# Performance work log

Hardware: AMD Instinct MI355X
Metric: run time of the kernel (lower is better)

The kernel has to match this reference:

```python
import jax, jax.numpy as jnp
import numpy as np

B, N, E, H = 2, 4096, 1024, 16
HD = E // H                      # head_dim = 64
R = 8                            # LoRA rank
LORA_SCALE = 16.0 / R            # alpha / r = 2.0
BUCKET_SIZES = (256, 64, 16)


def setup_inputs() -> dict:
    key = jax.random.key(0)
    ks = jax.random.split(key, 24)
    inp = {"x": jax.random.normal(ks[0], (B, N, E), jnp.float32)}
    inp["wb_coarse"] = jax.random.randint(ks[1], (B, N), 0, 16)
    inp["wb_mid"] = jax.random.randint(ks[2], (B, N), 0, 64)
    inp["wb_fine"] = jax.random.randint(ks[3], (B, N), 0, 256)
    i = 4
    for name in ("q", "k", "v", "o"):
        inp[f"W{name}"] = jax.random.normal(ks[i], (E, E), jnp.float32) / np.sqrt(E); i += 1
        inp[f"b{name}"] = jax.random.normal(ks[i], (E,), jnp.float32) * 0.01; i += 1
        inp[f"A{name}"] = jax.random.normal(ks[i], (R, E), jnp.float32) / np.sqrt(E); i += 1
        inp[f"B{name}"] = jax.random.normal(ks[i], (E, R), jnp.float32) * 0.01; i += 1
    return inp


def _lora(x, W, b, A, Bm):
    # F.linear(x, W, b) + scale * x @ A.T @ B.T   (dropout=0 in eval)
    return x @ W.T + b + LORA_SCALE * ((x @ A.T) @ Bm.T)


def _chunked_attn(q, k, v, bidx, C):
    # q,k,v: [BH, N, D]; bidx: [BH, N] int; C: chunk size (divides N)
    BH, Nn, D = q.shape
    sidx = jnp.argsort(bidx, axis=1)
    uidx = jnp.argsort(sidx, axis=1)
    g = lambda t, i: jnp.take_along_axis(t, i[..., None], axis=1)
    qs, ks_, vs = g(q, sidx), g(k, sidx), g(v, sidx)
    nc = Nn // C
    qs = qs.reshape(BH, nc, C, D)
    ks_ = ks_.reshape(BH, nc, C, D)
    vs = vs.reshape(BH, nc, C, D)
    # previous chunk (look-back of one chunk); chunk 0 has no previous -> masked
    k_prev = jnp.concatenate([jnp.zeros_like(ks_[:, :1]), ks_[:, :-1]], axis=1)
    v_prev = jnp.concatenate([jnp.zeros_like(vs[:, :1]), vs[:, :-1]], axis=1)
    k_cat = jnp.concatenate([k_prev, ks_], axis=2)   # [BH, nc, 2C, D]
    v_cat = jnp.concatenate([v_prev, vs], axis=2)
    scores = jnp.einsum('bncd,bnkd->bnck', qs, k_cat) / jnp.sqrt(jnp.asarray(D, qs.dtype))
    # mask look-back keys for chunk 0 (torch path attends only within chunk 0)
    chunk_ids = jnp.arange(nc)[:, None, None]        # [nc,1,1]
    key_pos = jnp.arange(2 * C)[None, None, :]       # [1,1,2C]
    neg = jnp.finfo(scores.dtype).min
    scores = jnp.where((chunk_ids == 0) & (key_pos < C), neg, scores)
    attn = jax.nn.softmax(scores, axis=-1)
    out = jnp.einsum('bnck,bnkd->bncd', attn, v_cat).reshape(BH, Nn, D)
    return jnp.take_along_axis(out, uidx[..., None], axis=1)


def reference(x, wb_coarse, wb_mid, wb_fine,
              Wq, bq, Aq, Bq, Wk, bk, Ak, Bk,
              Wv, bv, Av, Bv, Wo, bo, Ao, Bo):
    q = _lora(x, Wq, bq, Aq, Bq)
    k = _lora(x, Wk, bk, Ak, Bk)
    v = _lora(x, Wv, bv, Av, Bv)
    to_heads = lambda t: t.reshape(B, N, H, HD).transpose(0, 2, 1, 3).reshape(B * H, N, HD)
    qh, kh, vh = to_heads(q), to_heads(k), to_heads(v)
    expand = lambda w: jnp.broadcast_to(w[:, None, :], (B, H, N)).reshape(B * H, N)
    wbs = (expand(wb_coarse), expand(wb_mid), expand(wb_fine))
    outs = (_chunked_attn(qh, kh, vh, wbs[0], BUCKET_SIZES[0])
            + _chunked_attn(qh, kh, vh, wbs[1], BUCKET_SIZES[1])
            + _chunked_attn(qh, kh, vh, wbs[2], BUCKET_SIZES[2])) / 3.0
    outs = outs.reshape(B, H, N, HD).transpose(0, 2, 1, 3).reshape(B, N, E)
    return _lora(outs, Wo, bo, Ao, Bo)
```

## Files before the change

kernel.cpp:

```cpp
#include <hip/hip_runtime.h>
#include <cstdint>
#include <cstddef>

#define BDIM 2
#define NTOK 4096
#define EDIM 1024
#define HEADS 16
#define HDIM 64
#define MROWS (BDIM * NTOK)

typedef unsigned short u16;
typedef __attribute__((ext_vector_type(8))) short bf16x8;
typedef __attribute__((ext_vector_type(8))) unsigned short u16x8;
typedef __attribute__((ext_vector_type(4))) float f32x4;

#define MFMA(a, b, c) __builtin_amdgcn_mfma_f32_16x16x32_bf16(a, b, c, 0, 0, 0)
#define BAR() asm volatile("s_barrier" ::: "memory")
#define SETPRIO(p) __builtin_amdgcn_s_setprio(p)

__device__ inline void split2(float x, u16& h, u16& l) {
    union { float f; unsigned u; } a;
    a.f = x;
    unsigned uh = a.u + 0x7fff + ((a.u >> 16) & 1);
    h = (u16)(uh >> 16);
    union { unsigned u; float f; } hf; hf.u = (unsigned)h << 16;
    a.f = x - hf.f;
    unsigned ul = a.u + 0x7fff + ((a.u >> 16) & 1);
    l = (u16)(ul >> 16);
}

__device__ inline u16 bf16rne(float x) {
    union { float f; unsigned u; } a; a.f = x;
    unsigned r = a.u + 0x7fff + ((a.u >> 16) & 1);
    return (u16)(r >> 16);
}

#define GLL(gp, lp) __builtin_amdgcn_global_load_lds( \
    (const __attribute__((address_space(1))) unsigned*)(gp), \
    (__attribute__((address_space(3))) unsigned*)(lp), 16, 0, 0)

__global__ __launch_bounds__(256) void build_weff4_kernel(
    const float* __restrict__ W0, const float* __restrict__ A0, const float* __restrict__ B0,
    const float* __restrict__ W1, const float* __restrict__ A1, const float* __restrict__ B1,
    const float* __restrict__ W2, const float* __restrict__ A2, const float* __restrict__ B2,
    const float* __restrict__ W3, const float* __restrict__ A3, const float* __restrict__ B3,
    u16* __restrict__ dh0, u16* __restrict__ dl0,
    u16* __restrict__ dh1, u16* __restrict__ dl1,
    u16* __restrict__ dh2, u16* __restrict__ dl2,
    u16* __restrict__ dh3, u16* __restrict__ dl3)
{
    int s = blockIdx.y;
    const float* W = (s == 0) ? W0 : (s == 1) ? W1 : (s == 2) ? W2 : W3;
    const float* A = (s == 0) ? A0 : (s == 1) ? A1 : (s == 2) ? A2 : A3;
    const float* Bm = (s == 0) ? B0 : (s == 1) ? B1 : (s == 2) ? B2 : B3;
    u16* dh = (s == 0) ? dh0 : (s == 1) ? dh1 : (s == 2) ? dh2 : dh3;
    u16* dl = (s == 0) ? dl0 : (s == 1) ? dl1 : (s == 2) ? dl2 : dl3;

    int idx = blockIdx.x * 256 + threadIdx.x;
    int o = idx >> 10, i = idx & 1023;
    float sum = 0.f;
#pragma unroll
    for (int r = 0; r < 8; ++r) sum += Bm[o * 8 + r] * A[r * 1024 + i];
    float w = W[idx] + 2.0f * sum;
    u16 h, l;
    split2(w, h, l);
    dh[idx] = h; dl[idx] = l;
}

__global__ __launch_bounds__(256) void split_kernel(
    const float* __restrict__ src, u16* __restrict__ dh, u16* __restrict__ dl)
{
    int idx = blockIdx.x * 256 + threadIdx.x;
    float4 v = ((const float4*)src)[idx];
    ushort4 h, l;
    split2(v.x, h.x, l.x);
    split2(v.y, h.y, l.y);
    split2(v.z, h.z, l.z);
    split2(v.w, h.w, l.w);
    ((ushort4*)dh)[idx] = h;
    ((ushort4*)dl)[idx] = l;
}

__global__ __launch_bounds__(256) void sumsplit3_kernel(
    const float* __restrict__ A, const float* __restrict__ B,
    const float* __restrict__ Cc, u16* __restrict__ dh, u16* __restrict__ dl)
{
    int idx = blockIdx.x * 256 + threadIdx.x;
    float4 a = ((const float4*)A)[idx];
    float4 b = ((const float4*)B)[idx];
    float4 c = ((const float4*)Cc)[idx];
    float v[4] = {(a.x + b.x) + c.x, (a.y + b.y) + c.y,
                  (a.z + b.z) + c.z, (a.w + b.w) + c.w};
    ushort4 h, l;
    split2(v[0], h.x, l.x);
    split2(v[1], h.y, l.y);
    split2(v[2], h.z, l.z);
    split2(v[3], h.w, l.w);
    ((ushort4*)dh)[idx] = h;
    ((ushort4*)dl)[idx] = l;
}

__global__ __launch_bounds__(256) void sort3_kernel(
    const int* __restrict__ w0, const int* __restrict__ w1,
    const int* __restrict__ w2, int* __restrict__ sidx)
{
    __shared__ int sb[NTOK];
    __shared__ int cnt[32][256];
    __shared__ int gb[256];
    const int* srcs[3] = {w0, w1, w2};
    int t = threadIdx.x;
    const int* w = srcs[blockIdx.y] + blockIdx.x * NTOK;
    int* outp = sidx + ((int)blockIdx.y * BDIM + (int)blockIdx.x) * NTOK;

    for (int i = t; i < NTOK; i += 256) sb[i] = w[i];
    for (int i = t; i < 32 * 256; i += 256) ((int*)cnt)[i] = 0;
    __syncthreads();

    int g = t >> 3;
#pragma unroll
    for (int e = 0; e < 16; ++e)
        atomicAdd(&cnt[g][sb[g * 128 + (t & 7) + 8 * e]], 1);
    __syncthreads();

    int run = 0;
#pragma unroll
    for (int gg = 0; gg < 32; ++gg) {
        int c = cnt[gg][t];
        cnt[gg][t] = run;
        run += c;
    }
    gb[t] = run;
    __syncthreads();
    if (t == 0) {
        int acc = 0;
        for (int v = 0; v < 256; ++v) { int c = gb[v]; gb[v] = acc; acc += c; }
    }
    __syncthreads();
    for (int i = t; i < 32 * 256; i += 256) {
        int v = i & 255, gg = i >> 8;
        cnt[gg][v] += gb[v];
    }
    __syncthreads();

    if (t < 32) {
        int base = t * 128;
        for (int e = 0; e < 128; ++e) {
            int v = sb[base + e];
            int p = cnt[t][v]++;
            outp[p] = base + e;
        }
    }
}

__global__ __launch_bounds__(512, 2) void gemm_qk_kernel(
    const u16* __restrict__ Xh, const u16* __restrict__ Xl,
    const u16* __restrict__ Wh, const u16* __restrict__ Wl,
    const float* __restrict__ bq, const float* __restrict__ bk,
    u16* __restrict__ qh, u16* __restrict__ ql,
    u16* __restrict__ kh, u16* __restrict__ kl)
{
    __shared__ __align__(16) unsigned char smem[147456];
    u16* lds = (u16*)smem;
    const int PA_h = 0, PA_l = 8192, PB_h = 16384, PB_l = 20480;

    int t = threadIdx.x;
    int lane = t & 63, wave = t >> 6;
    int bid = blockIdx.x;
    int wg = (bid & 7) * 64 + (bid >> 3);
    int bx = wg & 15, by = wg >> 4;
    int m0 = by * 256, n0 = bx * 128;

    int lrow = lane & 15, lq = lane >> 4;
    size_t aoff = (size_t)(m0 + wave * 32 + lrow) * EDIM + lq * 8;
    size_t boff = (size_t)(n0 + wave * 16 + lrow) * EDIM + lq * 8;
    int slabA = wave * 2;
    int sA0 = (wave >> 1) * 4;
    int sB0 = (wave & 1) * 4;
    f32x4 acc[4][4] = {};

#pragma unroll
    for (int tt = 0; tt < 2; ++tt) {
        u16* sbuf = lds + tt * 24576;
        int kk = tt * 32;
        GLL(Xh + aoff + kk,             sbuf + PA_h + (slabA + 0) * 512);
        GLL(Xh + aoff + kk + 16 * EDIM, sbuf + PA_h + (slabA + 1) * 512);
        GLL(Xl + aoff + kk,             sbuf + PA_l + (slabA + 0) * 512);
        GLL(Xl + aoff + kk + 16 * EDIM, sbuf + PA_l + (slabA + 1) * 512);
        GLL(Wh + boff + kk, sbuf + PB_h + wave * 512);
        GLL(Wl + boff + kk, sbuf + PB_l + wave * 512);
    }
    asm volatile("s_waitcnt vmcnt(6)" ::: "memory");
    BAR();

    for (int t32 = 0; t32 < 32; ++t32) {
        u16* rb = lds + (t32 % 3) * 24576;
        u16* sbuf = lds + ((t32 + 2) % 3) * 24576;
        bool pf = (t32 + 2) < 32;
        int kn = (t32 + 2) * 32;
        bf16x8 bhf[4], blf[4];
#pragma unroll
        for (int p = 0; p < 4; ++p) {
            if (p == 0) {
// ... 4 lines not shown
                }
            }
            bf16x8 aph = *(const bf16x8*)(rb + PA_h + (sA0 + p) * 512 + lane * 8);
            bf16x8 apl = *(const bf16x8*)(rb + PA_l + (sA0 + p) * 512 + lane * 8);
            if (pf) {
                if (p == 0) {
                    GLL(Xh + aoff + kn,             sbuf + PA_h + (slabA + 0) * 512);
                    GLL(Xh + aoff + kn + 16 * EDIM, sbuf + PA_h + (slabA + 1) * 512);
                } else if (p == 1) {
                    GLL(Xl + aoff + kn,             sbuf + PA_l + (slabA + 0) * 512);
                    GLL(Xl + aoff + kn + 16 * EDIM, sbuf + PA_l + (slabA + 1) * 512);
                } else if (p == 2) {
                    GLL(Wh + boff + kn, sbuf + PB_h + wave * 512);
                    GLL(Wl + boff + kn, sbuf + PB_l + wave * 512);
                }
            }
            BAR();
            SETPRIO(1);
#pragma unroll
            for (int j = 0; j < 4; ++j) {
                acc[p][j] = MFMA(aph, bhf[j], acc[p][j]);
                acc[p][j] = MFMA(aph, blf[j], acc[p][j]);
                acc[p][j] = MFMA(apl, bhf[j], acc[p][j]);
            }
            SETPRIO(0);
            if (p == 3) {
                if (pf) asm volatile("s_waitcnt vmcnt(6)" ::: "memory");
                else    asm volatile("s_waitcnt vmcnt(0)" ::: "memory");
            }
            BAR();
        }
    }

    int proj = n0 >> 10;
    const float* bias = proj ? bk : bq;
    u16* ohp = proj ? kh : qh;
    u16* olp = proj ? kl : ql;
    int wm = (wave >> 1) * 64, wn = (wave & 1) * 64;
    int q4 = lane >> 4, l16 = lane & 15;
    int cb = (n0 & 1023) + wn;
    float bj[4];
#pragma unroll
    for (int j = 0; j < 4; ++j) bj[j] = bias[cb + j * 16 + l16];
    float* repw = (float*)smem + wave * 2176;
    int r8 = lane >> 3, c8 = lane & 7;
#pragma unroll
    for (int gph = 0; gph < 2; ++gph) {
#pragma unroll
        for (int ii = 0; ii < 2; ++ii)
#pragma unroll
            for (int j = 0; j < 4; ++j)
#pragma unroll
                for (int r = 0; r < 4; ++r)
                    repw[(ii * 16 + q4 * 4 + r) * 68 + j * 16 + l16] =
                        acc[gph * 2 + ii][j][r] + bj[j];
#pragma unroll
        for (int rg = 0; rg < 4; ++rg) {
            int lr = rg * 8 + r8;
            float4 f0 = *(float4*)(repw + lr * 68 + c8 * 8);
            float4 f1 = *(float4*)(repw + lr * 68 + c8 * 8 + 4);
            float fa[8] = {f0.x, f0.y, f0.z, f0.w, f1.x, f1.y, f1.z, f1.w};
            size_t off = (size_t)(m0 + wm + gph * 32 + lr) * EDIM + cb + c8 * 8;
            u16x8 hv, lv;
#pragma unroll
            for (int e = 0; e < 8; ++e) {
                float v = fa[e];
                if (proj == 0) v *= 0.125f;
                u16 hh, ll;
                split2(v, hh, ll);
                hv[e] = hh; lv[e] = ll;
            }
            *(u16x8*)(ohp + off) = hv;
            *(u16x8*)(olp + off) = lv;
        }
    }
}

__global__ __launch_bounds__(512, 2) void gemm_v_kernel(
    const u16* __restrict__ Xh, const u16* __restrict__ Wv,
    const float* __restrict__ bv, u16* __restrict__ vh)
{
    __shared__ __align__(16) unsigned char smem[73728];
    u16* lds = (u16*)smem;

    int t = threadIdx.x;
    int lane = t & 63, wave = t >> 6;
    int bid = blockIdx.x;
    int wg = (bid & 7) * 32 + (bid >> 3);
    int bx = wg & 7, by = wg >> 3;
    int m0 = by * 256, nc0 = bx * 128;

    int lrow = lane & 15, lq = lane >> 4;
    size_t aoff = (size_t)(m0 + wave * 32 + lrow) * EDIM + lq * 8;
    size_t boff = (size_t)(nc0 + wave * 16 + lrow) * EDIM + lq * 8;
    int slabA = wave * 2;
    int sA0 = (wave >> 1) * 4;
    int sB0 = (wave & 1) * 4;
    f32x4 acc[4][4] = {};

#pragma unroll
    for (int tt = 0; tt < 2; ++tt) {
        u16* sbuf = lds + tt * 12288;
        int kk = tt * 32;
        GLL(Xh + aoff + kk,             sbuf + (slabA + 0) * 512);
        GLL(Xh + aoff + kk + 16 * EDIM, sbuf + (slabA + 1) * 512);
        GLL(Wv + boff + kk,             sbuf + 8192 + wave * 512);
    }
    asm volatile("s_waitcnt vmcnt(3)" ::: "memory");
    BAR();

    for (int t32 = 0; t32 < 32; ++t32) {
        u16* rb = lds + (t32 % 3) * 12288;
        u16* sbuf = lds + ((t32 + 2) % 3) * 12288;
        bool pf = (t32 + 2) < 32;
        int kn = (t32 + 2) * 32;

        bf16x8 bhf[4];
#pragma unroll
        for (int j = 0; j < 4; ++j)
            bhf[j] = *(const bf16x8*)(rb + 8192 + (sB0 + j) * 512 + lane * 8);
        bf16x8 a0 = *(const bf16x8*)(rb + (sA0 + 0) * 512 + lane * 8);
        bf16x8 a1 = *(const bf16x8*)(rb + (sA0 + 1) * 512 + lane * 8);
        if (pf) {
            GLL(Xh + aoff + kn,             sbuf + (slabA + 0) * 512);
            GLL(Xh + aoff + kn + 16 * EDIM, sbuf + (slabA + 1) * 512);
        }
        BAR();
        SETPRIO(1);
#pragma unroll
        for (int j = 0; j < 4; ++j) {
            acc[0][j] = MFMA(a0, bhf[j], acc[0][j]);
            acc[1][j] = MFMA(a1, bhf[j], acc[1][j]);
        }
        SETPRIO(0);
        BAR();

        bf16x8 a2 = *(const bf16x8*)(rb + (sA0 + 2) * 512 + lane * 8);
        bf16x8 a3 = *(const bf16x8*)(rb + (sA0 + 3) * 512 + lane * 8);
        if (pf) GLL(Wv + boff + kn, sbuf + 8192 + wave * 512);
        BAR();
        SETPRIO(1);
#pragma unroll
        for (int j = 0; j < 4; ++j) {
            acc[2][j] = MFMA(a2, bhf[j], acc[2][j]);
            acc[3][j] = MFMA(a3, bhf[j], acc[3][j]);
        }
        SETPRIO(0);
        if (pf) asm volatile("s_waitcnt vmcnt(3)" ::: "memory");
        else    asm volatile("s_waitcnt vmcnt(0)" ::: "memory");
        BAR();
    }

    int wm = (wave >> 1) * 64, wn = (wave & 1) * 64;
    int q4 = lane >> 4, l16 = lane & 15;
    int cb = nc0 + wn;
    float bj[4];
#pragma unroll
    for (int j = 0; j < 4; ++j) bj[j] = bv[cb + j * 16 + l16];
    float* repw = (float*)smem + wave * 2176;
    int r8 = lane >> 3, c8 = lane & 7;
#pragma unroll
    for (int gph = 0; gph < 2; ++gph) {
#pragma unroll
        for (int ii = 0; ii < 2; ++ii)
#pragma unroll
            for (int j = 0; j < 4; ++j)
#pragma unroll
                for (int r = 0; r < 4; ++r)
                    repw[(ii * 16 + q4 * 4 + r) * 68 + j * 16 + l16] =
                        acc[gph * 2 + ii][j][r] + bj[j];
#pragma unroll
        for (int rg = 0; rg < 4; ++rg) {
            int lr = rg * 8 + r8;
            float4 f0 = *(float4*)(repw + lr * 68 + c8 * 8);
            float4 f1 = *(float4*)(repw + lr * 68 + c8 * 8 + 4);
            float fa[8] = {f0.x, f0.y, f0.z, f0.w, f1.x, f1.y, f1.z, f1.w};
            size_t off = (size_t)(m0 + wm + gph * 32 + lr) * EDIM + cb + c8 * 8;
            u16x8 hv;
#pragma unroll
            for (int e = 0; e < 8; ++e) hv[e] = bf16rne(fa[e]);
            *(u16x8*)(vh + off) = hv;
        }
    }
}

__global__ __launch_bounds__(512, 2) void gemm_o_kernel(
    const u16* __restrict__ Xh, const u16* __restrict__ Xl,
    const u16* __restrict__ Wh, const u16* __restrict__ Wl,
    const float* __restrict__ bias, float* __restrict__ Y)
{
    __shared__ __align__(16) unsigned char smem[147456];
    u16* lds = (u16*)smem;
    const int PA_h = 0, PA_l = 8192, PB_h = 16384, PB_l = 20480;

    int t = threadIdx.x;
    int lane = t & 63, wave = t >> 6;
    int bid = blockIdx.x;
    int wg = (bid & 7) * 32 + (bid >> 3);
    int bx = wg & 7, by = wg >> 3;
    int m0 = by * 256, n0 = bx * 128;

    int lrow = lane & 15, lq = lane >> 4;
    size_t aoff = (size_t)(m0 + wave * 32 + lrow) * EDIM + lq * 8;
    size_t boff = (size_t)(n0 + wave * 16 + lrow) * EDIM + lq * 8;
    int slabA = wave * 2;
    int sA0 = (wave >> 1) * 4;
    int sB0 = (wave & 1) * 4;
    f32x4 acc[4][4] = {};

#pragma unroll
    for (int tt = 0; tt < 2; ++tt) {
        u16* sbuf = lds + tt * 24576;
        int kk = tt * 32;
        GLL(Xh + aoff + kk,             sbuf + PA_h + (slabA + 0) * 512);
        GLL(Xh + aoff + kk + 16 * EDIM, sbuf + PA_h + (slabA + 1) * 512);
        GLL(Xl + aoff + kk,             sbuf + PA_l + (slabA + 0) * 512);
        GLL(Xl + aoff + kk + 16 * EDIM, sbuf + PA_l + (slabA + 1) * 512);
        GLL(Wh + boff + kk, sbuf + PB_h + wave * 512);
        GLL(Wl + boff + kk, sbuf + PB_l + wave * 512);
    }
    asm volatile("s_waitcnt vmcnt(6)" ::: "memory");
    BAR();

    for (int t32 = 0; t32 < 32; ++t32) {
        u16* rb = lds + (t32 % 3) * 24576;
        u16* sbuf = lds + ((t32 + 2) % 3) * 24576;
        bool pf = (t32 + 2) < 32;
        int kn = (t32 + 2) * 32;
        bf16x8 bhf[4], blf[4];
#pragma unroll
        for (int p = 0; p < 4; ++p) {
            if (p == 0) {
#pragma unroll
                for (int j = 0; j < 4; ++j) {
                    bhf[j] = *(const bf16x8*)(rb + PB_h + (sB0 + j) * 512 + lane * 8);
                    blf[j] = *(const bf16x8*)(rb + PB_l + (sB0 + j) * 512 + lane * 8);
                }
            }
            bf16x8 aph = *(const bf16x8*)(rb + PA_h + (sA0 + p) * 512 + lane * 8);
            bf16x8 apl = *(const bf16x8*)(rb + PA_l + (sA0 + p) * 512 + lane * 8);
            if (pf) {
                if (p == 0) {
                    GLL(Xh + aoff + kn,             sbuf + PA_h + (slabA + 0) * 512);
                    GLL(Xh + aoff + kn + 16 * EDIM, sbuf + PA_h + (slabA + 1) * 512);
                } else if (p == 1) {
                    GLL(Xl + aoff + kn,             sbuf + PA_l + (slabA + 0) * 512);
                    GLL(Xl + aoff + kn + 16 * EDIM, sbuf + PA_l + (slabA + 1) * 512);
                } else if (p == 2) {
                    GLL(Wh + boff + kn, sbuf + PB_h + wave * 512);
                    GLL(Wl + boff + kn, sbuf + PB_l + wave * 512);
                }
            }
            BAR();
            SETPRIO(1);
#pragma unroll
            for (int j = 0; j < 4; ++j) {
                acc[p][j] = MFMA(aph, bhf[j], acc[p][j]);
                acc[p][j] = MFMA(aph, blf[j], acc[p][j]);
                acc[p][j] = MFMA(apl, bhf[j], acc[p][j]);
            }
            SETPRIO(0);
            if (p == 3) {
                if (pf) asm volatile("s_waitcnt vmcnt(6)" ::: "memory");
                else    asm volatile("s_waitcnt vmcnt(0)" ::: "memory");
            }
            BAR();
        }
    }

    int wm = (wave >> 1) * 64, wn = (wave & 1) * 64;
    int col_in = lane & 15, rquad = lane >> 4;
#pragma unroll
    for (int j = 0; j < 4; ++j) {
        int col = n0 + wn + j * 16 + col_in;
        float bvv = bias[col];
#pragma unroll
        for (int i = 0; i < 4; ++i) {
            int mbase = m0 + wm + i * 16 + rquad * 4;
#pragma unroll
            for (int r = 0; r < 4; ++r)
                Y[(size_t)(mbase + r) * EDIM + col] = acc[i][j][r] + bvv;
        }
    }
}

template <int MODE>
__global__ __launch_bounds__(256, 3) void attn_mfma_kernel(
    const u16* __restrict__ Qh, const u16* __restrict__ Ql,
    const u16* __restrict__ Kh, const u16* __restrict__ Kl,
    const u16* __restrict__ Vh, const int* __restrict__ sidx_base, int zofs,
    float* __restrict__ out0, float* __restrict__ out1, float* __restrict__ out2,
    u16* __restrict__ osh, u16* __restrict__ osl)
{
    __shared__ u16 KfH[2][4096], KfL[2][4096];
    __shared__ u16 VL[64 * 72];
    __shared__ u16 PbH[4 * 16 * 56];

    int bx_, bh_, bz_;
    if (MODE == 0 && gridDim.z == 3) {
        int lid = blockIdx.x + (blockIdx.y << 5) + (blockIdx.z << 10);
        int xcd = lid & 7, j = lid >> 3;
        bh_ = xcd + 8 * (j / 96);
        int rem = j % 96;
        bz_ = rem >> 5;
        bx_ = rem & 31;
    } else {
        bx_ = blockIdx.x; bh_ = blockIdx.y; bz_ = blockIdx.z;
    }

    int sidx_i = bz_ + zofs;
    int lgC = 8 - 2 * sidx_i;
    const int* sxb = sidx_base + sidx_i * BDIM * NTOK;
    float* out = (sidx_i == 0) ? out0 : (sidx_i == 1) ? out1 : out2;

    int t = threadIdx.x;
    int lane = t & 63, wave = t >> 6;
    int quad = lane >> 4, l16 = lane & 15;
    int b = bh_ >> 4, h = bh_ & 15;
    int p0 = bx_ * 128;
    sxb += b * NTOK;

    int ptile[2], ws_[2], we_[2];
    bf16x8 qhf[2][2], qlf[2][2];
#pragma unroll
    for (int tq = 0; tq < 2; ++tq) {
        ptile[tq] = p0 + wave * 32 + tq * 16;
        int c = ptile[tq] >> lgC;
        ws_[tq] = (c > 0) ? (c - 1) << lgC : 0;
        we_[tq] = (c + 1) << lgC;
// ... 101 lines not shown
                        sa = MFMA(qhf[tq][1], kl0[1], sa);
                        sa = MFMA(qlf[tq][1], kh0[1], sa);
                    }
                    if (v1) {
                        sb2 = MFMA(qhf[tq][0], kh1[0], sb2);
                        sb2 = MFMA(qhf[tq][0], kl1[0], sb2);
                        sb2 = MFMA(qlf[tq][0], kh1[0], sb2);
                        sb2 = MFMA(qhf[tq][1], kh1[1], sb2);
                        sb2 = MFMA(qhf[tq][1], kl1[1], sb2);
                        sb2 = MFMA(qlf[tq][1], kh1[1], sb2);
                    }
                    SETPRIO(0);
                    float smax = -1e30f;
                    if (v0) smax = fmaxf(smax, fmaxf(fmaxf(sa[0], sa[1]), fmaxf(sa[2], sa[3])));
                    if (v1) smax = fmaxf(smax, fmaxf(fmaxf(sb2[0], sb2[1]), fmaxf(sb2[2], sb2[3])));
                    smax = fmaxf(smax, __shfl_xor(smax, 1));
                    smax = fmaxf(smax, __shfl_xor(smax, 2));
                    smax = fmaxf(smax, __shfl_xor(smax, 4));
                    smax = fmaxf(smax, __shfl_xor(smax, 8));
                    float mold = mrun[tq];
                    float mnew = mold;
                    if (smax > mold + 8.0f) {
                        mnew = smax;
                        mrun[tq] = mnew;
                        float alpha = __expf(mold - mnew);
#pragma unroll
                        for (int r = 0; r < 4; ++r) lpart[tq][r] *= alpha;
#pragma unroll
                        for (int dt = 0; dt < 4; ++dt) {
                            oacc[tq][dt][0] *= alpha; oacc[tq][dt][1] *= alpha;
                            oacc[tq][dt][2] *= alpha; oacc[tq][dt][3] *= alpha;
                        }
                    }
                    u16* pbh = PbH + wave * 896;
#pragma unroll
                    for (int r = 0; r < 4; ++r) {
                        float pa = v0 ? __expf(sa[r] - mnew) : 0.f;
                        float pbv = v1 ? __expf(sb2[r] - mnew) : 0.f;
                        lpart[tq][r] += pa + pbv;
                        pbh[(quad * 4 + r) * 56 + l16] = bf16rne(pa);
                        pbh[(quad * 4 + r) * 56 + 16 + l16] = bf16rne(pbv);
                    }
                    bf16x8 ph = *(const bf16x8*)(pbh + l16 * 56 + quad * 8);
                    int kh2 = g0 >> 5;
                    SETPRIO(1);
#pragma unroll
                    for (int dt = 0; dt < 4; ++dt) {
                        bf16x8 vv = *(const bf16x8*)(VL + (dt * 16 + l16) * 72 + kh2 * 32 + quad * 8);
                        oacc[tq][dt] = MFMA(ph, vv, oacc[tq][dt]);
                    }
                    SETPRIO(0);
                }
            }
        }

        asm volatile("s_waitcnt vmcnt(0)" ::: "memory");
        __syncthreads();
        if (pf) {
#pragma unroll
            for (int it = 0; it < 2; ++it) {
                int c = it * 256 + t;
                int key = c & 63, dg = c >> 6;
#pragma unroll
                for (int e = 0; e < 8; ++e)
                    VL[(dg * 8 + e) * 72 + key] = (u16)vreg[it][e];
            }
        }
        __syncthreads();
        pb ^= 1;
    }

#pragma unroll
    for (int tq = 0; tq < 2; ++tq) {
        float inv[4];
#pragma unroll
        for (int r = 0; r < 4; ++r) {
// ... 38 lines not shown
    const int*   wbc = (const int*)d_in[1];
    const int*   wbm = (const int*)d_in[2];
    const int*   wbf = (const int*)d_in[3];
    const float* Wq = (const float*)d_in[4],  *bq = (const float*)d_in[5];
    const float* Aq = (const float*)d_in[6],  *Bq = (const float*)d_in[7];
    const float* Wk = (const float*)d_in[8],  *bk = (const float*)d_in[9];
    const float* Ak = (const float*)d_in[10], *Bk = (const float*)d_in[11];
    const float* Wv = (const float*)d_in[12], *bv = (const float*)d_in[13];
    const float* Av = (const float*)d_in[14], *Bv = (const float*)d_in[15];
    const float* Wo = (const float*)d_in[16], *bo = (const float*)d_in[17];
    const float* Ao = (const float*)d_in[18], *Bo = (const float*)d_in[19];

    const size_t EE  = (size_t)EDIM * EDIM;
    const size_t BNE = (size_t)MROWS * EDIM;

    char* wsb = (char*)d_ws;
    float* ab = (float*)wsb;                        wsb += BNE * 4;
    u16* xh = (u16*)wsb;                            wsb += BNE * 2;
    u16* xl = (u16*)wsb;                            wsb += BNE * 2;
    u16* qh = (u16*)wsb;                            wsb += BNE * 2;
    u16* ql = (u16*)wsb;                            wsb += BNE * 2;
    u16* kh = (u16*)wsb;                            wsb += BNE * 2;
    u16* kl = (u16*)wsb;                            wsb += BNE * 2;
    u16* vh = (u16*)wsb;                            wsb += BNE * 2;
    u16* wh_all = (u16*)wsb;                        wsb += 3 * EE * 2;
    u16* wl_all = (u16*)wsb;                        wsb += 3 * EE * 2;
    u16* woh = (u16*)wsb;                           wsb += EE * 2;
    u16* wol = (u16*)wsb;                           wsb += EE * 2;
    int* sidx = (int*)wsb;                          wsb += 3 * BDIM * NTOK * 4;
    float* abC = (float*)wsb;
    size_t need3 = (size_t)(wsb - (char*)d_ws) + BNE * 4;
    bool merged = (ws_size >= need3);

    split_kernel<<<BNE / 1024, 256, 0, stream>>>(x, xh, xl);

    build_weff4_kernel<<<dim3(4096, 4), 256, 0, stream>>>(
        Wq, Aq, Bq, Wk, Ak, Bk, Wv, Av, Bv, Wo, Ao, Bo,
        wh_all + 0 * EE, wl_all + 0 * EE,
        wh_all + 1 * EE, wl_all + 1 * EE,
        wh_all + 2 * EE, wl_all + 2 * EE,
        woh, wol);

    sort3_kernel<<<dim3(BDIM, 3), 256, 0, stream>>>(wbc, wbm, wbf, sidx);

    gemm_qk_kernel<<<512, 512, 0, stream>>>(xh, xl, wh_all, wl_all,
                                            bq, bk, qh, ql, kh, kl);
    gemm_v_kernel<<<256, 512, 0, stream>>>(xh, wh_all + 2 * EE, bv, vh);

    if (merged) {
        float* abB = (float*)xh;
        dim3 ga3(NTOK / 128, BDIM * HEADS, 3);
        attn_mfma_kernel<0><<<ga3, 256, 0, stream>>>(
            qh, ql, kh, kl, vh, sidx, 0, ab, abB, abC, nullptr, nullptr);
        sumsplit3_kernel<<<BNE / 1024, 256, 0, stream>>>(ab, abB, abC, qh, ql);
        gemm_o_kernel<<<256, 512, 0, stream>>>(qh, ql, woh, wol, bo, (float*)d_out);
    } else {
        dim3 ga(NTOK / 128, BDIM * HEADS);
        attn_mfma_kernel<0><<<ga, 256, 0, stream>>>(
            qh, ql, kh, kl, vh, sidx, 0, ab, ab, ab, nullptr, nullptr);
        attn_mfma_kernel<1><<<ga, 256, 0, stream>>>(
            qh, ql, kh, kl, vh, sidx, 1, ab, ab, ab, nullptr, nullptr);
        attn_mfma_kernel<2><<<ga, 256, 0, stream>>>(
            qh, ql, kh, kl, vh, sidx, 2, ab, ab, ab, xh, xl);
        gemm_o_kernel<<<256, 512, 0, stream>>>(xh, xl, woh, wol, bo, (float*)d_out);
    }
}
```

Before: 477.3 us.

## Merge prep kernels and QK/V GEMMs into single launches; pad per-tile P buffer

Folds the x split, LoRA weight build and bucket sort into one prep kernel dispatched by block index, and fuses the Q/K split-precision GEMM and the V GEMM into one launch. The intent is to cut launch overhead and let the sort blocks and the V tiles run alongside the other work instead of serialising, and to reduce tail effects. The attention kernel's P staging buffer is resized to give each tq its own slot with a 40-element row stride, which changes the LDS bank mapping and removes reuse of one buffer across tq. The fused GEMM kernel carries the larger register and LDS footprint of the Q/K path for the V blocks too, and V blocks scheduled first may unbalance work.

Result: no change. 469.2 us, median of 2 (-1.7%).

```diff
diff --git a/kernel.cpp b/kernel.cpp
--- a/kernel.cpp
+++ b/kernel.cpp
@@ -39,7 +39,10 @@
     (const __attribute__((address_space(1))) unsigned*)(gp), \
     (__attribute__((address_space(3))) unsigned*)(lp), 16, 0, 0)
 
-__global__ __launch_bounds__(256) void build_weff4_kernel(
+__global__ __launch_bounds__(256) void prep_kernel(
+    const float* __restrict__ x, u16* __restrict__ xh, u16* __restrict__ xl,
+    const int* __restrict__ w0, const int* __restrict__ w1,
+    const int* __restrict__ w2, int* __restrict__ sidx,
     const float* __restrict__ W0, const float* __restrict__ A0, const float* __restrict__ B0,
     const float* __restrict__ W1, const float* __restrict__ A1, const float* __restrict__ B1,
     const float* __restrict__ W2, const float* __restrict__ A2, const float* __restrict__ B2,
@@ -49,36 +52,85 @@
     u16* __restrict__ dh2, u16* __restrict__ dl2,
     u16* __restrict__ dh3, u16* __restrict__ dl3)
 {
-    int s = blockIdx.y;
-    const float* W = (s == 0) ? W0 : (s == 1) ? W1 : (s == 2) ? W2 : W3;
-    const float* A = (s == 0) ? A0 : (s == 1) ? A1 : (s == 2) ? A2 : A3;
-    const float* Bm = (s == 0) ? B0 : (s == 1) ? B1 : (s == 2) ? B2 : B3;
-    u16* dh = (s == 0) ? dh0 : (s == 1) ? dh1 : (s == 2) ? dh2 : dh3;
-    u16* dl = (s == 0) ? dl0 : (s == 1) ? dl1 : (s == 2) ? dl2 : dl3;
-
-    int idx = blockIdx.x * 256 + threadIdx.x;
-    int o = idx >> 10, i = idx & 1023;
-    float sum = 0.f;
-#pragma unroll
-    for (int r = 0; r < 8; ++r) sum += Bm[o * 8 + r] * A[r * 1024 + i];
-    float w = W[idx] + 2.0f * sum;
-    u16 h, l;
-    split2(w, h, l);
-    dh[idx] = h; dl[idx] = l;
-}
-
-__global__ __launch_bounds__(256) void split_kernel(
-    const float* __restrict__ src, u16* __restrict__ dh, u16* __restrict__ dl)
-{
-    int idx = blockIdx.x * 256 + threadIdx.x;
-    float4 v = ((const float4*)src)[idx];
-    ushort4 h, l;
-    split2(v.x, h.x, l.x);
-    split2(v.y, h.y, l.y);
-    split2(v.z, h.z, l.z);
-    split2(v.w, h.w, l.w);
-    ((ushort4*)dh)[idx] = h;
-    ((ushort4*)dl)[idx] = l;
+    __shared__ int sb[NTOK];
+    __shared__ int cnt[32][256];
+    __shared__ int gb[256];
+    int bid = blockIdx.x;
+    int t = threadIdx.x;
+
+    if (bid < 6) {
+        int by = bid >> 1, bx = bid & 1;
+        const int* srcs[3] = {w0, w1, w2};
+        const int* w = srcs[by] + bx * NTOK;
+        int* outp = sidx + ((int)by * BDIM + (int)bx) * NTOK;
+
+        for (int i = t; i < NTOK; i += 256) sb[i] = w[i];
+        for (int i = t; i < 32 * 256; i += 256) ((int*)cnt)[i] = 0;
+        __syncthreads();
+
+        int g = t >> 3;
+#pragma unroll
+        for (int e = 0; e < 16; ++e)
+            atomicAdd(&cnt[g][sb[g * 128 + (t & 7) + 8 * e]], 1);
+        __syncthreads();
+
+        int run = 0;
+#pragma unroll
+        for (int gg = 0; gg < 32; ++gg) {
+            int c = cnt[gg][t];
+            cnt[gg][t] = run;
+            run += c;
+        }
+        gb[t] = run;
+        __syncthreads();
+        if (t == 0) {
+            int acc = 0;
+            for (int v = 0; v < 256; ++v) { int c = gb[v]; gb[v] = acc; acc += c; }
+        }
+        __syncthreads();
+        for (int i = t; i < 32 * 256; i += 256) {
+            int v = i & 255, gg = i >> 8;
+            cnt[gg][v] += gb[v];
+        }
+        __syncthreads();
+
+        if (t < 32) {
+            int base = t * 128;
+            for (int e = 0; e < 128; ++e) {
+                int v = sb[base + e];
+                int p = cnt[t][v]++;
+                outp[p] = base + e;
+            }
+        }
+    } else if (bid < 8198) {
+        int idx = (bid - 6) * 256 + t;
+        float4 v = ((const float4*)x)[idx];
+        ushort4 h, l;
+        split2(v.x, h.x, l.x);
+        split2(v.y, h.y, l.y);
+        split2(v.z, h.z, l.z);
+        split2(v.w, h.w, l.w);
+        ((ushort4*)xh)[idx] = h;
+        ((ushort4*)xl)[idx] = l;
+    } else {
+        int wid = bid - 8198;
+        int s = wid >> 12, bx = wid & 4095;
+        const float* W = (s == 0) ? W0 : (s == 1) ? W1 : (s == 2) ? W2 : W3;
+        const float* A = (s == 0) ? A0 : (s == 1) ? A1 : (s == 2) ? A2 : A3;
+        const float* Bm = (s == 0) ? B0 : (s == 1) ? B1 : (s == 2) ? B2 : B3;
+        u16* dh = (s == 0) ? dh0 : (s == 1) ? dh1 : (s == 2) ? dh2 : dh3;
+        u16* dl = (s == 0) ? dl0 : (s == 1) ? dl1 : (s == 2) ? dl2 : dl3;
+
+        int idx = bx * 256 + t;
+        int o = idx >> 10, i = idx & 1023;
+        float sum = 0.f;
+#pragma unroll
+        for (int r = 0; r < 8; ++r) sum += Bm[o * 8 + r] * A[r * 1024 + i];
+        float w = W[idx] + 2.0f * sum;
+        u16 h, l;
+        split2(w, h, l);
+        dh[idx] = h; dl[idx] = l;
+    }
 }
 
 __global__ __launch_bounds__(256) void sumsplit3_kernel(
@@ -100,64 +152,256 @@
     ((ushort4*)dl)[idx] = l;
 }
 
-__global__ __launch_bounds__(256) void sort3_kernel(
-    const int* __restrict__ w0, const int* __restrict__ w1,
-    const int* __restrict__ w2, int* __restrict__ sidx)
+__global__ __launch_bounds__(256) void split_kernel(
+    const float* __restrict__ src, u16* __restrict__ dh, u16* __restrict__ dl)
 {
-    __shared__ int sb[NTOK];
-    __shared__ int cnt[32][256];
-    __shared__ int gb[256];
-    const int* srcs[3] = {w0, w1, w2};
-    int t = threadIdx.x;
-    const int* w = srcs[blockIdx.y] + blockIdx.x * NTOK;
-    int* outp = sidx + ((int)blockIdx.y * BDIM + (int)blockIdx.x) * NTOK;
-
-    for (int i = t; i < NTOK; i += 256) sb[i] = w[i];
-    for (int i = t; i < 32 * 256; i += 256) ((int*)cnt)[i] = 0;
-    __syncthreads();
-
-    int g = t >> 3;
-#pragma unroll
-    for (int e = 0; e < 16; ++e)
-        atomicAdd(&cnt[g][sb[g * 128 + (t & 7) + 8 * e]], 1);
-    __syncthreads();
-
-    int run = 0;
-#pragma unroll
-    for (int gg = 0; gg < 32; ++gg) {
-        int c = cnt[gg][t];
-        cnt[gg][t] = run;
-        run += c;
-    }
-    gb[t] = run;
-    __syncthreads();
-    if (t == 0) {
-        int acc = 0;
-        for (int v = 0; v < 256; ++v) { int c = gb[v]; gb[v] = acc; acc += c; }
-    }
-    __syncthreads();
-    for (int i = t; i < 32 * 256; i += 256) {
-        int v = i & 255, gg = i >> 8;
-        cnt[gg][v] += gb[v];
-    }
-    __syncthreads();
-
-    if (t < 32) {
-        int base = t * 128;
-        for (int e = 0; e < 128; ++e) {
-            int v = sb[base + e];
-            int p = cnt[t][v]++;
-            outp[p] = base + e;
-        }
-    }
+    int idx = blockIdx.x * 256 + threadIdx.x;
+    float4 v = ((const float4*)src)[idx];
+    ushort4 h, l;
+    split2(v.x, h.x, l.x);
+    split2(v.y, h.y, l.y);
+    split2(v.z, h.z, l.z);
+    split2(v.w, h.w, l.w);
+    ((ushort4*)dh)[idx] = h;
+    ((ushort4*)dl)[idx] = l;
 }
 
-__global__ __launch_bounds__(512, 2) void gemm_qk_kernel(
+__global__ __launch_bounds__(512, 2) void gemm_qkv_kernel(
     const u16* __restrict__ Xh, const u16* __restrict__ Xl,
     const u16* __restrict__ Wh, const u16* __restrict__ Wl,
+    const u16* __restrict__ Wvh,
     const float* __restrict__ bq, const float* __restrict__ bk,
+    const float* __restrict__ bv,
     u16* __restrict__ qh, u16* __restrict__ ql,
-    u16* __restrict__ kh, u16* __restrict__ kl)
+    u16* __restrict__ kh, u16* __restrict__ kl, u16* __restrict__ vh)
+{
+    __shared__ __align__(16) unsigned char smem[147456];
+    u16* lds = (u16*)smem;
+    int t = threadIdx.x;
+    int lane = t & 63, wave = t >> 6;
+    int bid = blockIdx.x;
+
+    if (bid < 256) {
+        int wg = (bid & 7) * 32 + (bid >> 3);
+        int bx = wg & 7, by = wg >> 3;
+        int m0 = by * 256, nc0 = bx * 128;
+
+        int lrow = lane & 15, lq = lane >> 4;
+        size_t aoff = (size_t)(m0 + wave * 32 + lrow) * EDIM + lq * 8;
+        size_t boff = (size_t)(nc0 + wave * 16 + lrow) * EDIM + lq * 8;
+        int slabA = wave * 2;
+        int sA0 = (wave >> 1) * 4;
+        int sB0 = (wave & 1) * 4;
+        f32x4 acc[4][4] = {};
+
+#pragma unroll
+        for (int tt = 0; tt < 2; ++tt) {
+            u16* sbuf = lds + tt * 12288;
+            int kk = tt * 32;
+            GLL(Xh + aoff + kk,             sbuf + (slabA + 0) * 512);
+            GLL(Xh + aoff + kk + 16 * EDIM, sbuf + (slabA + 1) * 512);
+            GLL(Wvh + boff + kk,            sbuf + 8192 + wave * 512);
+        }
+        asm volatile("s_waitcnt vmcnt(3)" ::: "memory");
+        BAR();
+
+        for (int t32 = 0; t32 < 32; ++t32) {
+            u16* rb = lds + (t32 % 3) * 12288;
+            u16* sbuf = lds + ((t32 + 2) % 3) * 12288;
+            bool pf = (t32 + 2) < 32;
+            int kn = (t32 + 2) * 32;
+
+            bf16x8 bhf[4];
+#pragma unroll
+            for (int j = 0; j < 4; ++j)
+                bhf[j] = *(const bf16x8*)(rb + 8192 + (sB0 + j) * 512 + lane * 8);
+            bf16x8 a0 = *(const bf16x8*)(rb + (sA0 + 0) * 512 + lane * 8);
+            bf16x8 a1 = *(const bf16x8*)(rb + (sA0 + 1) * 512 + lane * 8);
+            if (pf) {
+                GLL(Xh + aoff + kn,             sbuf + (slabA + 0) * 512);
+                GLL(Xh + aoff + kn + 16 * EDIM, sbuf + (slabA + 1) * 512);
+            }
+            BAR();
+            SETPRIO(1);
+#pragma unroll
+            for (int j = 0; j < 4; ++j) {
+                acc[0][j] = MFMA(a0, bhf[j], acc[0][j]);
+                acc[1][j] = MFMA(a1, bhf[j], acc[1][j]);
+            }
+            SETPRIO(0);
+            BAR();
+
+            bf16x8 a2 = *(const bf16x8*)(rb + (sA0 + 2) * 512 + lane * 8);
+            bf16x8 a3 = *(const bf16x8*)(rb + (sA0 + 3) * 512 + lane * 8);
+            if (pf) GLL(Wvh + boff + kn, sbuf + 8192 + wave * 512);
+            BAR();
+            SETPRIO(1);
+#pragma unroll
+            for (int j = 0; j < 4; ++j) {
+                acc[2][j] = MFMA(a2, bhf[j], acc[2][j]);
+                acc[3][j] = MFMA(a3, bhf[j], acc[3][j]);
+            }
+            SETPRIO(0);
+            if (pf) asm volatile("s_waitcnt vmcnt(3)" ::: "memory");
+            else    asm volatile("s_waitcnt vmcnt(0)" ::: "memory");
+            BAR();
+        }
+
+        int wm = (wave >> 1) * 64, wn = (wave & 1) * 64;
+        int q4 = lane >> 4, l16 = lane & 15;
+        int cb = nc0 + wn;
+        float bj[4];
+#pragma unroll
+        for (int j = 0; j < 4; ++j) bj[j] = bv[cb + j * 16 + l16];
+        float* repw = (float*)smem + wave * 2176;
+        int r8 = lane >> 3, c8 = lane & 7;
+#pragma unroll
+        for (int gph = 0; gph < 2; ++gph) {
+#pragma unroll
+            for (int ii = 0; ii < 2; ++ii)
+#pragma unroll
+                for (int j = 0; j < 4; ++j)
+#pragma unroll
+                    for (int r = 0; r < 4; ++r)
+                        repw[(ii * 16 + q4 * 4 + r) * 68 + j * 16 + l16] =
+                            acc[gph * 2 + ii][j][r] + bj[j];
+#pragma unroll
+            for (int rg = 0; rg < 4; ++rg) {
+                int lr = rg * 8 + r8;
+                float4 f0 = *(float4*)(repw + lr * 68 + c8 * 8);
+                float4 f1 = *(float4*)(repw + lr * 68 + c8 * 8 + 4);
+                float fa[8] = {f0.x, f0.y, f0.z, f0.w, f1.x, f1.y, f1.z, f1.w};
+                size_t off = (size_t)(m0 + wm + gph * 32 + lr) * EDIM + cb + c8 * 8;
+                u16x8 hv;
+#pragma unroll
+                for (int e = 0; e < 8; ++e) hv[e] = bf16rne(fa[e]);
+                *(u16x8*)(vh + off) = hv;
+            }
+        }
+    } else {
+        const int PA_h = 0, PA_l = 8192, PB_h = 16384, PB_l = 20480;
+        int qidx = bid - 256;
+        int wg = (qidx & 7) * 64 + (qidx >> 3);
+        int bx = wg & 15, by = wg >> 4;
+        int m0 = by * 256, n0 = bx * 128;
+
+        int lrow = lane & 15, lq = lane >> 4;
+        size_t aoff = (size_t)(m0 + wave * 32 + lrow) * EDIM + lq * 8;
+        size_t boff = (size_t)(n0 + wave * 16 + lrow) * EDIM + lq * 8;
+        int slabA = wave * 2;
+        int sA0 = (wave >> 1) * 4;
+        int sB0 = (wave & 1) * 4;
+        f32x4 acc[4][4] = {};
+
+#pragma unroll
+        for (int tt = 0; tt < 2; ++tt) {
+            u16* sbuf = lds + tt * 24576;
+            int kk = tt * 32;
+            GLL(Xh + aoff + kk,             sbuf + PA_h + (slabA + 0) * 512);
+            GLL(Xh + aoff + kk + 16 * EDIM, sbuf + PA_h + (slabA + 1) * 512);
+            GLL(Xl + aoff + kk,             sbuf + PA_l + (slabA + 0) * 512);
+            GLL(Xl + aoff + kk + 16 * EDIM, sbuf + PA_l + (slabA + 1) * 512);
+            GLL(Wh + boff + kk, sbuf + PB_h + wave * 512);
+            GLL(Wl + boff + kk, sbuf + PB_l + wave * 512);
+        }
+        asm volatile("s_waitcnt vmcnt(6)" ::: "memory");
+        BAR();
+
+        for (int t32 = 0; t32 < 32; ++t32) {
+            u16* rb = lds + (t32 % 3) * 24576;
+            u16* sbuf = lds + ((t32 + 2) % 3) * 24576;
+            bool pf = (t32 + 2) < 32;
+            int kn = (t32 + 2) * 32;
+            bf16x8 bhf[4], blf[4];
+#pragma unroll
+            for (int p = 0; p < 4; ++p) {
+                if (p == 0) {
+#pragma unroll
+                    for (int j = 0; j < 4; ++j) {
+                        bhf[j] = *(const bf16x8*)(rb + PB_h + (sB0 + j) * 512 + lane * 8);
+                        blf[j] = *(const bf16x8*)(rb + PB_l + (sB0 + j) * 512 + lane * 8);
+                    }
+                }
+                bf16x8 aph = *(const bf16x8*)(rb + PA_h + (sA0 + p) * 512 + lane * 8);
+                bf16x8 apl = *(const bf16x8*)(rb + PA_l + (sA0 + p) * 512 + lane * 8);
+                if (pf) {
+                    if (p == 0) {
+                        GLL(Xh + aoff + kn,             sbuf + PA_h + (slabA + 0) * 512);
+                        GLL(Xh + aoff + kn + 16 * EDIM, sbuf + PA_h + (slabA + 1) * 512);
+                    } else if (p == 1) {
+                        GLL(Xl + aoff + kn,             sbuf + PA_l + (slabA + 0) * 512);
+                        GLL(Xl + aoff + kn + 16 * EDIM, sbuf + PA_l + (slabA + 1) * 512);
+                    } else if (p == 2) {
+                        GLL(Wh + boff + kn, sbuf + PB_h + wave * 512);
+                        GLL(Wl + boff + kn, sbuf + PB_l + wave * 512);
+                    }
+                }
+                BAR();
+                SETPRIO(1);
+#pragma unroll
+                for (int j = 0; j < 4; ++j) {
+                    acc[p][j] = MFMA(aph, bhf[j], acc[p][j]);
+                    acc[p][j] = MFMA(aph, blf[j], acc[p][j]);
+                    acc[p][j] = MFMA(apl, bhf[j], acc[p][j]);
+                }
+                SETPRIO(0);
+                if (p == 3) {
+                    if (pf) asm volatile("s_waitcnt vmcnt(6)" ::: "memory");
+                    else    asm volatile("s_waitcnt vmcnt(0)" ::: "memory");
+                }
+                BAR();
+            }
+        }
+
+        int proj = n0 >> 10;
+        const float* bias = proj ? bk : bq;
+        u16* ohp = proj ? kh : qh;
+        u16* olp = proj ? kl : ql;
+        int wm = (wave >> 1) * 64, wn = (wave & 1) * 64;
+        int q4 = lane >> 4, l16 = lane & 15;
+        int cb = (n0 & 1023) + wn;
+        float bj[4];
+#pragma unroll
+        for (int j = 0; j < 4; ++j) bj[j] = bias[cb + j * 16 + l16];
+        float* repw = (float*)smem + wave * 2176;
+        int r8 = lane >> 3, c8 = lane & 7;
+#pragma unroll
+        for (int gph = 0; gph < 2; ++gph) {
+#pragma unroll
+            for (int ii = 0; ii < 2; ++ii)
+#pragma unroll
+                for (int j = 0; j < 4; ++j)
+#pragma unroll
+                    for (int r = 0; r < 4; ++r)
+                        repw[(ii * 16 + q4 * 4 + r) * 68 + j * 16 + l16] =
+                            acc[gph * 2 + ii][j][r] + bj[j];
+#pragma unroll
+            for (int rg = 0; rg < 4; ++rg) {
+                int lr = rg * 8 + r8;
+                float4 f0 = *(float4*)(repw + lr * 68 + c8 * 8);
+                float4 f1 = *(float4*)(repw + lr * 68 + c8 * 8 + 4);
+                float fa[8] = {f0.x, f0.y, f0.z, f0.w, f1.x, f1.y, f1.z, f1.w};
+                size_t off = (size_t)(m0 + wm + gph * 32 + lr) * EDIM + cb + c8 * 8;
+                u16x8 hv, lv;
+#pragma unroll
+                for (int e = 0; e < 8; ++e) {
+                    float v = fa[e];
+                    if (proj == 0) v *= 0.125f;
+                    u16 hh, ll;
+                    split2(v, hh, ll);
+                    hv[e] = hh; lv[e] = ll;
+                }
+                *(u16x8*)(ohp + off) = hv;
+                *(u16x8*)(olp + off) = lv;
+            }
+        }
+    }
+}
+
+__global__ __launch_bounds__(512, 2) void gemm_o_kernel(
+    const u16* __restrict__ Xh, const u16* __restrict__ Xl,
+    const u16* __restrict__ Wh, const u16* __restrict__ Wl,
+    const float* __restrict__ bias, float* __restrict__ Y)
 {
     __shared__ __align__(16) unsigned char smem[147456];
     u16* lds = (u16*)smem;
@@ -166,8 +410,8 @@
     int t = threadIdx.x;
     int lane = t & 63, wave = t >> 6;
     int bid = blockIdx.x;
-    int wg = (bid & 7) * 64 + (bid >> 3);
-    int bx = wg & 15, by = wg >> 4;
+    int wg = (bid & 7) * 32 + (bid >> 3);
+    int bx = wg & 7, by = wg >> 3;
     int m0 = by * 256, n0 = bx * 128;
 
     int lrow = lane & 15, lq = lane >> 4;
@@ -238,242 +482,6 @@
         }
     }
 
-    int proj = n0 >> 10;
-    const float* bias = proj ? bk : bq;
-    u16* ohp = proj ? kh : qh;
-    u16* olp = proj ? kl : ql;
-    int wm = (wave >> 1) * 64, wn = (wave & 1) * 64;
-    int q4 = lane >> 4, l16 = lane & 15;
-    int cb = (n0 & 1023) + wn;
-    float bj[4];
-#pragma unroll
-    for (int j = 0; j < 4; ++j) bj[j] = bias[cb + j * 16 + l16];
-    float* repw = (float*)smem + wave * 2176;
-    int r8 = lane >> 3, c8 = lane & 7;
-#pragma unroll
-    for (int gph = 0; gph < 2; ++gph) {
-#pragma unroll
-        for (int ii = 0; ii < 2; ++ii)
-#pragma unroll
-            for (int j = 0; j < 4; ++j)
-#pragma unroll
-                for (int r = 0; r < 4; ++r)
-                    repw[(ii * 16 + q4 * 4 + r) * 68 + j * 16 + l16] =
-                        acc[gph * 2 + ii][j][r] + bj[j];
-#pragma unroll
-        for (int rg = 0; rg < 4; ++rg) {
-            int lr = rg * 8 + r8;
-            float4 f0 = *(float4*)(repw + lr * 68 + c8 * 8);
-            float4 f1 = *(float4*)(repw + lr * 68 + c8 * 8 + 4);
-            float fa[8] = {f0.x, f0.y, f0.z, f0.w, f1.x, f1.y, f1.z, f1.w};
-            size_t off = (size_t)(m0 + wm + gph * 32 + lr) * EDIM + cb + c8 * 8;
-            u16x8 hv, lv;
-#pragma unroll
-            for (int e = 0; e < 8; ++e) {
-                float v = fa[e];
-                if (proj == 0) v *= 0.125f;
-                u16 hh, ll;
-                split2(v, hh, ll);
-                hv[e] = hh; lv[e] = ll;
-            }
-            *(u16x8*)(ohp + off) = hv;
-            *(u16x8*)(olp + off) = lv;
-        }
-    }
-}
-
-__global__ __launch_bounds__(512, 2) void gemm_v_kernel(
-    const u16* __restrict__ Xh, const u16* __restrict__ Wv,
-    const float* __restrict__ bv, u16* __restrict__ vh)
-{
-    __shared__ __align__(16) unsigned char smem[73728];
-    u16* lds = (u16*)smem;
-
-    int t = threadIdx.x;
-    int lane = t & 63, wave = t >> 6;
-    int bid = blockIdx.x;
-    int wg = (bid & 7) * 32 + (bid >> 3);
-    int bx = wg & 7, by = wg >> 3;
-    int m0 = by * 256, nc0 = bx * 128;
-
-    int lrow = lane & 15, lq = lane >> 4;
-    size_t aoff = (size_t)(m0 + wave * 32 + lrow) * EDIM + lq * 8;
-    size_t boff = (size_t)(nc0 + wave * 16 + lrow) * EDIM + lq * 8;
-    int slabA = wave * 2;
-    int sA0 = (wave >> 1) * 4;
-    int sB0 = (wave & 1) * 4;
-    f32x4 acc[4][4] = {};
-
-#pragma unroll
-    for (int tt = 0; tt < 2; ++tt) {
-        u16* sbuf = lds + tt * 12288;
-        int kk = tt * 32;
-        GLL(Xh + aoff + kk,             sbuf + (slabA + 0) * 512);
-        GLL(Xh + aoff + kk + 16 * EDIM, sbuf + (slabA + 1) * 512);
-        GLL(Wv + boff + kk,             sbuf + 8192 + wave * 512);
-    }
-    asm volatile("s_waitcnt vmcnt(3)" ::: "memory");
-    BAR();
-
-    for (int t32 = 0; t32 < 32; ++t32) {
-        u16* rb = lds + (t32 % 3) * 12288;
-        u16* sbuf = lds + ((t32 + 2) % 3) * 12288;
-        bool pf = (t32 + 2) < 32;
-        int kn = (t32 + 2) * 32;
-
-        bf16x8 bhf[4];
-#pragma unroll
-        for (int j = 0; j < 4; ++j)
-            bhf[j] = *(const bf16x8*)(rb + 8192 + (sB0 + j) * 512 + lane * 8);
-        bf16x8 a0 = *(const bf16x8*)(rb + (sA0 + 0) * 512 + lane * 8);
-        bf16x8 a1 = *(const bf16x8*)(rb + (sA0 + 1) * 512 + lane * 8);
-        if (pf) {
-            GLL(Xh + aoff + kn,             sbuf + (slabA + 0) * 512);
-            GLL(Xh + aoff + kn + 16 * EDIM, sbuf + (slabA + 1) * 512);
-        }
-        BAR();
-        SETPRIO(1);
-#pragma unroll
-        for (int j = 0; j < 4; ++j) {
-            acc[0][j] = MFMA(a0, bhf[j], acc[0][j]);
-            acc[1][j] = MFMA(a1, bhf[j], acc[1][j]);
-        }
-        SETPRIO(0);
-        BAR();
-
-        bf16x8 a2 = *(const bf16x8*)(rb + (sA0 + 2) * 512 + lane * 8);
-        bf16x8 a3 = *(const bf16x8*)(rb + (sA0 + 3) * 512 + lane * 8);
-        if (pf) GLL(Wv + boff + kn, sbuf + 8192 + wave * 512);
-        BAR();
-        SETPRIO(1);
-#pragma unroll
-        for (int j = 0; j < 4; ++j) {
-            acc[2][j] = MFMA(a2, bhf[j], acc[2][j]);
-            acc[3][j] = MFMA(a3, bhf[j], acc[3][j]);
-        }
-        SETPRIO(0);
-        if (pf) asm volatile("s_waitcnt vmcnt(3)" ::: "memory");
-        else    asm volatile("s_waitcnt vmcnt(0)" ::: "memory");
-        BAR();
-    }
-
-    int wm = (wave >> 1) * 64, wn = (wave & 1) * 64;
-    int q4 = lane >> 4, l16 = lane & 15;
-    int cb = nc0 + wn;
-    float bj[4];
-#pragma unroll
-    for (int j = 0; j < 4; ++j) bj[j] = bv[cb + j * 16 + l16];
-    float* repw = (float*)smem + wave * 2176;
-    int r8 = lane >> 3, c8 = lane & 7;
-#pragma unroll
-    for (int gph = 0; gph < 2; ++gph) {
-#pragma unroll
-        for (int ii = 0; ii < 2; ++ii)
-#pragma unroll
-            for (int j = 0; j < 4; ++j)
-#pragma unroll
-                for (int r = 0; r < 4; ++r)
-                    repw[(ii * 16 + q4 * 4 + r) * 68 + j * 16 + l16] =
-                        acc[gph * 2 + ii][j][r] + bj[j];
-#pragma unroll
-        for (int rg = 0; rg < 4; ++rg) {
-            int lr = rg * 8 + r8;
-            float4 f0 = *(float4*)(repw + lr * 68 + c8 * 8);
-            float4 f1 = *(float4*)(repw + lr * 68 + c8 * 8 + 4);
-            float fa[8] = {f0.x, f0.y, f0.z, f0.w, f1.x, f1.y, f1.z, f1.w};
-            size_t off = (size_t)(m0 + wm + gph * 32 + lr) * EDIM + cb + c8 * 8;
-            u16x8 hv;
-#pragma unroll
-            for (int e = 0; e < 8; ++e) hv[e] = bf16rne(fa[e]);
-            *(u16x8*)(vh + off) = hv;
-        }
-    }
-}
-
-__global__ __launch_bounds__(512, 2) void gemm_o_kernel(
-    const u16* __restrict__ Xh, const u16* __restrict__ Xl,
-    const u16* __restrict__ Wh, const u16* __restrict__ Wl,
-    const float* __restrict__ bias, float* __restrict__ Y)
-{
-    __shared__ __align__(16) unsigned char smem[147456];
-    u16* lds = (u16*)smem;
-    const int PA_h = 0, PA_l = 8192, PB_h = 16384, PB_l = 20480;
-
-    int t = threadIdx.x;
-    int lane = t & 63, wave = t >> 6;
-    int bid = blockIdx.x;
-    int wg = (bid & 7) * 32 + (bid >> 3);
-    int bx = wg & 7, by = wg >> 3;
-    int m0 = by * 256, n0 = bx * 128;
-
-    int lrow = lane & 15, lq = lane >> 4;
-    size_t aoff = (size_t)(m0 + wave * 32 + lrow) * EDIM + lq * 8;
-    size_t boff = (size_t)(n0 + wave * 16 + lrow) * EDIM + lq * 8;
-    int slabA = wave * 2;
-    int sA0 = (wave >> 1) * 4;
-    int sB0 = (wave & 1) * 4;
-    f32x4 acc[4][4] = {};
-
-#pragma unroll
-    for (int tt = 0; tt < 2; ++tt) {
-        u16* sbuf = lds + tt * 24576;
-        int kk = tt * 32;
-        GLL(Xh + aoff + kk,             sbuf + PA_h + (slabA + 0) * 512);
-        GLL(Xh + aoff + kk + 16 * EDIM, sbuf + PA_h + (slabA + 1) * 512);
-        GLL(Xl + aoff + kk,             sbuf + PA_l + (slabA + 0) * 512);
-        GLL(Xl + aoff + kk + 16 * EDIM, sbuf + PA_l + (slabA + 1) * 512);
-        GLL(Wh + boff + kk, sbuf + PB_h + wave * 512);
-        GLL(Wl + boff + kk, sbuf + PB_l + wave * 512);
-    }
-    asm volatile("s_waitcnt vmcnt(6)" ::: "memory");
-    BAR();
-
-    for (int t32 = 0; t32 < 32; ++t32) {
-        u16* rb = lds + (t32 % 3) * 24576;
-        u16* sbuf = lds + ((t32 + 2) % 3) * 24576;
-        bool pf = (t32 + 2) < 32;
-        int kn = (t32 + 2) * 32;
-        bf16x8 bhf[4], blf[4];
-#pragma unroll
-        for (int p = 0; p < 4; ++p) {
-            if (p == 0) {
-#pragma unroll
-                for (int j = 0; j < 4; ++j) {
-                    bhf[j] = *(const bf16x8*)(rb + PB_h + (sB0 + j) * 512 + lane * 8);
-                    blf[j] = *(const bf16x8*)(rb + PB_l + (sB0 + j) * 512 + lane * 8);
-                }
-            }
-            bf16x8 aph = *(const bf16x8*)(rb + PA_h + (sA0 + p) * 512 + lane * 8);
-            bf16x8 apl = *(const bf16x8*)(rb + PA_l + (sA0 + p) * 512 + lane * 8);
-            if (pf) {
-                if (p == 0) {
-                    GLL(Xh + aoff + kn,             sbuf + PA_h + (slabA + 0) * 512);
-                    GLL(Xh + aoff + kn + 16 * EDIM, sbuf + PA_h + (slabA + 1) * 512);
-                } else if (p == 1) {
-                    GLL(Xl + aoff + kn,             sbuf + PA_l + (slabA + 0) * 512);
-                    GLL(Xl + aoff + kn + 16 * EDIM, sbuf + PA_l + (slabA + 1) * 512);
-                } else if (p == 2) {
-                    GLL(Wh + boff + kn, sbuf + PB_h + wave * 512);
-                    GLL(Wl + boff + kn, sbuf + PB_l + wave * 512);
-                }
-            }
-            BAR();
-            SETPRIO(1);
-#pragma unroll
-            for (int j = 0; j < 4; ++j) {
-                acc[p][j] = MFMA(aph, bhf[j], acc[p][j]);
-                acc[p][j] = MFMA(aph, blf[j], acc[p][j]);
-                acc[p][j] = MFMA(apl, bhf[j], acc[p][j]);
-            }
-            SETPRIO(0);
-            if (p == 3) {
-                if (pf) asm volatile("s_waitcnt vmcnt(6)" ::: "memory");
-                else    asm volatile("s_waitcnt vmcnt(0)" ::: "memory");
-            }
-            BAR();
-        }
-    }
-
     int wm = (wave >> 1) * 64, wn = (wave & 1) * 64;
     int col_in = lane & 15, rquad = lane >> 4;
 #pragma unroll
@@ -500,7 +508,7 @@
 {
     __shared__ u16 KfH[2][4096], KfL[2][4096];
     __shared__ u16 VL[64 * 72];
-    __shared__ u16 PbH[4 * 16 * 56];
+    __shared__ u16 PbH[4 * 2 * 16 * 40];
 
     int bx_, bh_, bz_;
     if (MODE == 0 && gridDim.z == 3) {
@@ -668,16 +676,16 @@
                             oacc[tq][dt][2] *= alpha; oacc[tq][dt][3] *= alpha;
                         }
                     }
-                    u16* pbh = PbH + wave * 896;
+                    u16* pbh = PbH + wave * 1280 + tq * 640;
 #pragma unroll
                     for (int r = 0; r < 4; ++r) {
                         float pa = v0 ? __expf(sa[r] - mnew) : 0.f;
                         float pbv = v1 ? __expf(sb2[r] - mnew) : 0.f;
                         lpart[tq][r] += pa + pbv;
-                        pbh[(quad * 4 + r) * 56 + l16] = bf16rne(pa);
-                        pbh[(quad * 4 + r) * 56 + 16 + l16] = bf16rne(pbv);
+                        pbh[(quad * 4 + r) * 40 + l16] = bf16rne(pa);
+                        pbh[(quad * 4 + r) * 40 + 16 + l16] = bf16rne(pbv);
                     }
-                    bf16x8 ph = *(const bf16x8*)(pbh + l16 * 56 + quad * 8);
+                    bf16x8 ph = *(const bf16x8*)(pbh + l16 * 40 + quad * 8);
                     int kh2 = g0 >> 5;
                     SETPRIO(1);
 #pragma unroll
@@ -782,20 +790,17 @@
     size_t need3 = (size_t)(wsb - (char*)d_ws) + BNE * 4;
     bool merged = (ws_size >= need3);
 
-    split_kernel<<<BNE / 1024, 256, 0, stream>>>(x, xh, xl);
-
-    build_weff4_kernel<<<dim3(4096, 4), 256, 0, stream>>>(
+    prep_kernel<<<24582, 256, 0, stream>>>(
+        x, xh, xl, wbc, wbm, wbf, sidx,
         Wq, Aq, Bq, Wk, Ak, Bk, Wv, Av, Bv, Wo, Ao, Bo,
         wh_all + 0 * EE, wl_all + 0 * EE,
         wh_all + 1 * EE, wl_all + 1 * EE,
         wh_all + 2 * EE, wl_all + 2 * EE,
         woh, wol);
 
-    sort3_kernel<<<dim3(BDIM, 3), 256, 0, stream>>>(wbc, wbm, wbf, sidx);
-
-    gemm_qk_kernel<<<512, 512, 0, stream>>>(xh, xl, wh_all, wl_all,
-                                            bq, bk, qh, ql, kh, kl);
-    gemm_v_kernel<<<256, 512, 0, stream>>>(xh, wh_all + 2 * EE, bv, vh);
+    gemm_qkv_kernel<<<768, 512, 0, stream>>>(
+        xh, xl, wh_all, wl_all, wh_all + 2 * EE,
+        bq, bk, bv, qh, ql, kh, kl, vh);
 
     if (merged) {
         float* abB = (float*)xh;
```
